# Kernel optimization log

Hardware: AMD Instinct MI355X
Metric: run time of the kernel (lower is better)

Reference implementation:

```python
import jax, jax.numpy as jnp
import numpy as np

B, H, S, D = 2, 16, 2048, 128  # batch, heads, seq_len, head_dim (hidden=2048, heads=16)


def setup_inputs() -> dict:
    key = jax.random.key(0)
    kq, kk, kv = jax.random.split(key, 3)
    q = jax.random.normal(kq, (B, H, S, D), dtype=jnp.float32)
    k = jax.random.normal(kk, (B, H, S, D), dtype=jnp.float32)
    v = jax.random.normal(kv, (B, H, S, D), dtype=jnp.float32)
    return {"q": q, "k": k, "v": v}


def reference(q, k, v):
    # scores = (q @ k^T) / sqrt(head_dim)  -> [B, H, S, S]
    scaling = 1.0 / jnp.sqrt(jnp.asarray(q.shape[-1], dtype=q.dtype))
    scores = jnp.einsum('bhqd,bhkd->bhqk', q, k) * scaling
    # softmax over keys (dropout p=0.0 -> identity in eval / p=0)
    weights = jax.nn.softmax(scores, axis=-1)
    # out = weights @ v -> [B, H, S, D]
    return jnp.einsum('bhqk,bhkd->bhqd', weights, v)
```

## Files before the change

### kernel.cpp

```cpp
#include <hip/hip_runtime.h>
#include <stdint.h>

typedef __attribute__((ext_vector_type(4))) float f32x4;
typedef __attribute__((ext_vector_type(16))) float f32x16;
typedef __attribute__((ext_vector_type(8))) short bf16x8;

constexpr int S_ = 2048;
constexpr int D_ = 128;
constexpr int BH = 32;
constexpr int KB = 64;
constexpr int NT = S_ / KB;
constexpr float QSCALE = 0.08838834764831845f * 1.4426950408889634f;

__device__ __forceinline__ short f2bf(float f) {
  uint32_t u = __float_as_uint(f);
  u += 0x7fffu + ((u >> 16) & 1u);
  return (short)(u >> 16);
}

__device__ __forceinline__ void gll16(const void* g, void* l) {
  __builtin_amdgcn_global_load_lds(
      (const __attribute__((address_space(1))) void*)g,
      (__attribute__((address_space(3))) void*)l, 16, 0, 0);
}

__global__ void prep_k(const float* __restrict__ k, short* __restrict__ kb) {
  const size_t N8 = (size_t)BH * S_ * D_ / 8;
  size_t i = (size_t)blockIdx.x * blockDim.x + threadIdx.x;
  const size_t stride = (size_t)gridDim.x * blockDim.x;
  for (; i < N8; i += stride) {
    float4 a = reinterpret_cast<const float4*>(k)[i * 2];
    float4 b = reinterpret_cast<const float4*>(k)[i * 2 + 1];
    bf16x8 o;
    o[0] = f2bf(a.x); o[1] = f2bf(a.y); o[2] = f2bf(a.z); o[3] = f2bf(a.w);
    o[4] = f2bf(b.x); o[5] = f2bf(b.y); o[6] = f2bf(b.z); o[7] = f2bf(b.w);
    reinterpret_cast<bf16x8*>(kb)[i] = o;
  }
}

__global__ void prep_vt(const float* __restrict__ v, short* __restrict__ vt) {
  __shared__ __align__(16) short Lt[64][136];
  const int bh = blockIdx.x >> 5;
  const int s0 = (blockIdx.x & 31) * 64;
  const int t = threadIdx.x;
#pragma unroll
  for (int i = 0; i < 4; ++i) {
    int g = t + 256 * i;
    int r = g >> 4, c8 = g & 15;
    const float* src = v + ((size_t)bh * S_ + s0 + r) * D_ + c8 * 8;
    float4 f0 = *reinterpret_cast<const float4*>(src);
    float4 f1 = *reinterpret_cast<const float4*>(src + 4);
    bf16x8 o;
    o[0] = f2bf(f0.x); o[1] = f2bf(f0.y); o[2] = f2bf(f0.z); o[3] = f2bf(f0.w);
    o[4] = f2bf(f1.x); o[5] = f2bf(f1.y); o[6] = f2bf(f1.z); o[7] = f2bf(f1.w);
    *reinterpret_cast<bf16x8*>(&Lt[r][c8 * 8]) = o;
  }
  __syncthreads();
#pragma unroll
  for (int i = 0; i < 4; ++i) {
    int g = t * 4 + i;
    int d = g >> 3, s8 = g & 7;
    bf16x8 o;
#pragma unroll
    for (int j = 0; j < 8; ++j) o[j] = Lt[s8 * 8 + j][d];
    *reinterpret_cast<bf16x8*>(&vt[((size_t)bh * D_ + d) * S_ + s0 + s8 * 8]) = o;
  }
}

__global__ __launch_bounds__(512, 2) void attn_fwd_v8(
    const float* __restrict__ q, const short* __restrict__ kbf,
    const short* __restrict__ vt, float* __restrict__ out)
{
  __shared__ __align__(16) short Klds[2][8192];
  __shared__ __align__(16) short Vlds[3][8192];

  const int lid = blockIdx.x;
  const int swz = (lid & 7) * 32 + (lid >> 3);
  const int qt = swz & 7;
  const int bh = swz >> 3;

  const int tid = threadIdx.x;
  const int wid = tid >> 6;
  const int lane = tid & 63;
  const int l32 = lane & 31;
  const int hi = lane >> 5;

  const int qrow = qt * 256 + wid * 32 + l32;

  bf16x8 bq[8];
  {
    const float* qg_ = q + ((size_t)bh * S_ + qrow) * D_ + hi * 8;
#pragma unroll
    for (int s = 0; s < 8; ++s) {
      float4 f0 = *reinterpret_cast<const float4*>(qg_ + s * 16);
      float4 f1 = *reinterpret_cast<const float4*>(qg_ + s * 16 + 4);
      bf16x8 a;
      a[0] = f2bf(f0.x * QSCALE); a[1] = f2bf(f0.y * QSCALE);
      a[2] = f2bf(f0.z * QSCALE); a[3] = f2bf(f0.w * QSCALE);
      a[4] = f2bf(f1.x * QSCALE); a[5] = f2bf(f1.y * QSCALE);
      a[6] = f2bf(f1.z * QSCALE); a[7] = f2bf(f1.w * QSCALE);
      bq[s] = a;
    }
  }

  const short* kg = kbf + (size_t)bh * S_ * D_;
  const short* vg = vt + (size_t)bh * D_ * S_;

  int kofs[2], vofs[2];
#pragma unroll
  for (int j = 0; j < 2; ++j) {
    const int g = wid * 2 + j;
    kofs[j] = lane * D_ + g * 8;
    const int G = g * 64 + lane;
    vofs[j] = (G & 127) * S_ + (G >> 7) * 8;
  }
  auto stage = [&](int t) {
    const short* ks = kg + (size_t)(t * KB) * D_;
    const short* vs = vg + t * KB;
    short* kd = &Klds[t & 1][wid * 1024];
    short* vd = &Vlds[t % 3][wid * 1024];
    gll16(ks + kofs[0], kd);
    gll16(ks + kofs[1], kd + 512);
    gll16(vs + vofs[0], vd);
    gll16(vs + vofs[1], vd + 512);
  };

  f32x16 oacc[4], loacc;
#pragma unroll
  for (int d0 = 0; d0 < 4; ++d0)
#pragma unroll
    for (int r = 0; r < 16; ++r) oacc[d0][r] = 0.f;
#pragma unroll
  for (int r = 0; r < 16; ++r) loacc[r] = 0.f;

  union { uint32_t u[4]; bf16x8 b; } onesu;
#pragma unroll
  for (int i = 0; i < 4; ++i) onesu.u[i] = 0x3F803F80u;

  bf16x8 pfrag[4];

  stage(0);
  for (int t = 0; t < NT; ++t) {
    __syncthreads();
    if (t + 1 < NT) stage(t + 1);

    const short* Kb = &Klds[t & 1][0];

    f32x16 sf0, sf1;
#pragma unroll
    for (int r = 0; r < 16; ++r) { sf0[r] = 0.f; sf1[r] = 0.f; }
    __builtin_amdgcn_s_setprio(1);
#pragma unroll
    for (int s = 0; s < 8; ++s) {
      bf16x8 a0 = *reinterpret_cast<const bf16x8*>(&Kb[((s * 2 + hi) * 64 + l32) * 8]);
      bf16x8 a1 = *reinterpret_cast<const bf16x8*>(&Kb[((s * 2 + hi) * 64 + 32 + l32) * 8]);
      sf0 = __builtin_amdgcn_mfma_f32_32x32x16_bf16(a0, bq[s], sf0, 0, 0, 0);
      sf1 = __builtin_amdgcn_mfma_f32_32x32x16_bf16(a1, bq[s], sf1, 0, 0, 0);
    }
    __builtin_amdgcn_s_setprio(0);

    if (t > 0) {
      const short* Vp = &Vlds[(t + 2) % 3][0];
      __builtin_amdgcn_s_setprio(1);
#pragma unroll
      for (int ks2 = 0; ks2 < 4; ++ks2) {
#pragma unroll
        for (int d0 = 0; d0 < 4; ++d0) {
          bf16x8 av = *reinterpret_cast<const bf16x8*>(
              &Vp[((ks2 * 2 + hi) * 128 + d0 * 32 + l32) * 8]);
          oacc[d0] = __builtin_amdgcn_mfma_f32_32x32x16_bf16(av, pfrag[ks2], oacc[d0], 0, 0, 0);
        }
        loacc = __builtin_amdgcn_mfma_f32_32x32x16_bf16(onesu.b, pfrag[ks2], loacc, 0, 0, 0);
      }
      __builtin_amdgcn_s_setprio(0);
    }

#define MAKE_P(SF, F0)                                                          \
    {                                                                           \
      uint32_t w[8];                                                            \
      _Pragma("unroll")                                                         \
      for (int i2 = 0; i2 < 8; ++i2) {                                          \
        float e0 = exp2f(SF[2 * i2]);                                           \
        float e1 = exp2f(SF[2 * i2 + 1]);                                       \
        asm("v_cvt_pk_bf16_f32 %0, %1, %2" : "=v"(w[i2]) : "v"(e0), "v"(e1));   \
      }                                                                         \
      asm("v_permlane32_swap_b32 %0, %1" : "+v"(w[0]), "+v"(w[2]));             \
      asm("v_permlane32_swap_b32 %0, %1" : "+v"(w[1]), "+v"(w[3]));             \
      asm("v_permlane32_swap_b32 %0, %1" : "+v"(w[4]), "+v"(w[6]));             \
      asm("v_permlane32_swap_b32 %0, %1" : "+v"(w[5]), "+v"(w[7]));             \
      union { int4 i4; bf16x8 b; } u0, u1;                                      \
      u0.i4 = (int4){(int)w[0], (int)w[1], (int)w[2], (int)w[3]};               \
      u1.i4 = (int4){(int)w[4], (int)w[5], (int)w[6], (int)w[7]};               \
      pfrag[F0] = u0.b; pfrag[F0 + 1] = u1.b;                                   \
    }
    MAKE_P(sf0, 0)
    MAKE_P(sf1, 2)
#undef MAKE_P
  }

  {
    const short* Vp = &Vlds[(NT - 1) % 3][0];
    __builtin_amdgcn_s_setprio(1);
#pragma unroll
    for (int ks2 = 0; ks2 < 4; ++ks2) {
#pragma unroll
      for (int d0 = 0; d0 < 4; ++d0) {
        bf16x8 av = *reinterpret_cast<const bf16x8*>(
            &Vp[((ks2 * 2 + hi) * 128 + d0 * 32 + l32) * 8]);
        oacc[d0] = __builtin_amdgcn_mfma_f32_32x32x16_bf16(av, pfrag[ks2], oacc[d0], 0, 0, 0);
      }
      loacc = __builtin_amdgcn_mfma_f32_32x32x16_bf16(onesu.b, pfrag[ks2], loacc, 0, 0, 0);
    }
    __builtin_amdgcn_s_setprio(0);
  }

  const float inv = 1.0f / loacc[0];
  float* ob = out + ((size_t)bh * S_ + qrow) * D_;
#pragma unroll
  for (int d0 = 0; d0 < 4; ++d0)
#pragma unroll
    for (int r2 = 0; r2 < 4; ++r2) {
      float4 o4 = {oacc[d0][r2 * 4 + 0] * inv, oacc[d0][r2 * 4 + 1] * inv,
                   oacc[d0][r2 * 4 + 2] * inv, oacc[d0][r2 * 4 + 3] * inv};
      *reinterpret_cast<float4*>(ob + d0 * 32 + r2 * 8 + hi * 4) = o4;
    }
}

__global__ __launch_bounds__(256, 4) void attn_fwd_v1(
    const float* __restrict__ q, const float* __restrict__ k,
    const float* __restrict__ v, float* __restrict__ out)
{
  __shared__ __align__(16) short Klds[32 * 128];
  __shared__ __align__(16) short Vlds[128 * 40];
  __shared__ __align__(16) short Plds[4][16 * 40];
  const int lid = blockIdx.x;
  const int swz = (lid & 7) * 128 + (lid >> 3);
  const int qt = swz & 31;
  const int bh = swz >> 5;
  const int tid = threadIdx.x;
  const int wid = tid >> 6;
  const int lane = tid & 63;
  const int l16 = lane & 15;
  const int lhi = lane >> 4;
  const int qrow0 = qt * 64 + wid * 16;
  const float* qg = q + ((size_t)bh * S_ + qrow0 + l16) * D_;
  const float* kg = k + (size_t)bh * S_ * D_;
  const float* vg = v + (size_t)bh * S_ * D_;
  bf16x8 aq[4];
#pragma unroll
  for (int ks = 0; ks < 4; ++ks) {
    const float* p = qg + ks * 32 + lhi * 8;
    float4 f0 = *reinterpret_cast<const float4*>(p);
    float4 f1 = *reinterpret_cast<const float4*>(p + 4);
    bf16x8 a;
    a[0] = f2bf(f0.x * QSCALE); a[1] = f2bf(f0.y * QSCALE);
    a[2] = f2bf(f0.z * QSCALE); a[3] = f2bf(f0.w * QSCALE);
    a[4] = f2bf(f1.x * QSCALE); a[5] = f2bf(f1.y * QSCALE);
    a[6] = f2bf(f1.z * QSCALE); a[7] = f2bf(f1.w * QSCALE);
    aq[ks] = a;
  }
  float mrow[4], lrow[4];
  f32x4 oacc[8];
#pragma unroll
  for (int r = 0; r < 4; ++r) { mrow[r] = -1e30f; lrow[r] = 0.f; }
#pragma unroll
  for (int i = 0; i < 8; ++i) oacc[i] = (f32x4){0.f, 0.f, 0.f, 0.f};
  for (int t = 0; t < S_ / 32; ++t) {
    const int kv0 = t * 32;
    __syncthreads();
#pragma unroll
    for (int i = 0; i < 2; ++i) {
      const int g = tid * 2 + i;
      const int row = g >> 4;
      const int c8 = g & 15;
      const float* ksrc = kg + (size_t)(kv0 + row) * D_ + c8 * 8;
      float4 f0 = *reinterpret_cast<const float4*>(ksrc);
      float4 f1 = *reinterpret_cast<const float4*>(ksrc + 4);
      bf16x8 kk;
      kk[0] = f2bf(f0.x); kk[1] = f2bf(f0.y); kk[2] = f2bf(f0.z); kk[3] = f2bf(f0.w);
      kk[4] = f2bf(f1.x); kk[5] = f2bf(f1.y); kk[6] = f2bf(f1.z); kk[7] = f2bf(f1.w);
      *reinterpret_cast<bf16x8*>(
          &Klds[row * D_ + ((c8 * 8) ^ ((row & 7) << 3))]) = kk;
      const float* vsrc = vg + (size_t)(kv0 + row) * D_ + c8 * 8;
      float4 g0 = *reinterpret_cast<const float4*>(vsrc);
      float4 g1 = *reinterpret_cast<const float4*>(vsrc + 4);
      const int dbase = c8 * 8;
      Vlds[(dbase + 0) * 40 + row] = f2bf(g0.x);
      Vlds[(dbase + 1) * 40 + row] = f2bf(g0.y);
      Vlds[(dbase + 2) * 40 + row] = f2bf(g0.z);
      Vlds[(dbase + 3) * 40 + row] = f2bf(g0.w);
      Vlds[(dbase + 4) * 40 + row] = f2bf(g1.x);
      Vlds[(dbase + 5) * 40 + row] = f2bf(g1.y);
      Vlds[(dbase + 6) * 40 + row] = f2bf(g1.z);
      Vlds[(dbase + 7) * 40 + row] = f2bf(g1.w);
    }
    __syncthreads();
    f32x4 sfrag[2];
#pragma unroll
    for (int kb = 0; kb < 2; ++kb) {
      f32x4 acc = (f32x4){0.f, 0.f, 0.f, 0.f};
#pragma unroll
      for (int ks = 0; ks < 4; ++ks) {
        const int rowk = kb * 16 + l16;
        bf16x8 bk = *reinterpret_cast<const bf16x8*>(
            &Klds[rowk * D_ + (((ks * 4 + lhi) * 8) ^ ((rowk & 7) << 3))]);
        acc = __builtin_amdgcn_mfma_f32_16x16x32_bf16(aq[ks], bk, acc, 0, 0, 0);
      }
      sfrag[kb] = acc;
    }
    float mt[4];
#pragma unroll
    for (int r = 0; r < 4; ++r) mt[r] = fmaxf(sfrag[0][r], sfrag[1][r]);
#pragma unroll
    for (int off = 1; off < 16; off <<= 1)
#pragma unroll
      for (int r = 0; r < 4; ++r) mt[r] = fmaxf(mt[r], __shfl_xor(mt[r], off, 64));
    float al[4], ps[4];
#pragma unroll
    for (int r = 0; r < 4; ++r) {
      float mn = fmaxf(mrow[r], mt[r]);
      al[r] = exp2f(mrow[r] - mn);
      mrow[r] = mn;
      ps[r] = 0.f;
    }
#pragma unroll
    for (int kb = 0; kb < 2; ++kb)
#pragma unroll
      for (int r = 0; r < 4; ++r) {
        float p = exp2f(sfrag[kb][r] - mrow[r]);
        ps[r] += p;
        Plds[wid][(lhi * 4 + r) * 40 + kb * 16 + l16] = f2bf(p);
      }
#pragma unroll
    for (int off = 1; off < 16; off <<= 1)
#pragma unroll
      for (int r = 0; r < 4; ++r) ps[r] += __shfl_xor(ps[r], off, 64);
#pragma unroll
    for (int r = 0; r < 4; ++r) lrow[r] = lrow[r] * al[r] + ps[r];
#pragma unroll
    for (int i = 0; i < 8; ++i)
#pragma unroll
      for (int r = 0; r < 4; ++r) oacc[i][r] *= al[r];
    bf16x8 ap = *reinterpret_cast<const bf16x8*>(&Plds[wid][l16 * 40 + lhi * 8]);
#pragma unroll
    for (int d0 = 0; d0 < 8; ++d0) {
      bf16x8 bv = *reinterpret_cast<const bf16x8*>(
          &Vlds[(d0 * 16 + l16) * 40 + lhi * 8]);
      oacc[d0] = __builtin_amdgcn_mfma_f32_16x16x32_bf16(ap, bv, oacc[d0], 0, 0, 0);
    }
  }
#pragma unroll
  for (int r = 0; r < 4; ++r) {
    float inv = 1.0f / lrow[r];
    float* orow = out + ((size_t)bh * S_ + qrow0 + lhi * 4 + r) * D_ + l16;
#pragma unroll
    for (int d0 = 0; d0 < 8; ++d0) orow[d0 * 16] = oacc[d0][r] * inv;
  }
}

extern "C" void kernel_launch(void* const* d_in, const int* in_sizes, int n_in,
                              void* d_out, int out_size, void* d_ws, size_t ws_size,
                              hipStream_t stream) {
  (void)in_sizes; (void)n_in; (void)out_size;
  const float* q = (const float*)d_in[0];
  const float* k = (const float*)d_in[1];
  const float* v = (const float*)d_in[2];
  float* o = (float*)d_out;
  const size_t NEL = (size_t)BH * S_ * D_;
  const size_t need = NEL * 2 * sizeof(short);
  if (ws_size >= need) {
    short* kb = (short*)d_ws;
    short* vt = kb + NEL;
    hipLaunchKernelGGL(prep_k, dim3(2048), dim3(256), 0, stream, k, kb);
    hipLaunchKernelGGL(prep_vt, dim3(1024), dim3(256), 0, stream, v, vt);
    hipLaunchKernelGGL(attn_fwd_v8, dim3(256), dim3(512), 0, stream, q, kb, vt, o);
  } else {
    hipLaunchKernelGGL(attn_fwd_v1, dim3(1024), dim3(256), 0, stream, q, k, v, o);
  }
}
```

Measured before the change: 126.0 us.

## Halve attention workgroups to 4 waves and stagger PV/QK order across waves

The attention kernel now runs 512 workgroups of 256 threads (4 waves, 128 query rows each) instead of 256 workgroups of 512 threads. Each wave issues twice as many async global-to-LDS loads per tile. The loop barrier is replaced by an explicit vmcnt(0) wait plus s_barrier with scheduling fences. Odd waves do the P·V MFMA block before the QK^T block and even waves after it, so matrix and exp work from different waves can interleave. In exchange, K/V tiles are loaded into LDS twice as often in total, since each workgroup covers fewer query rows, and LDS use per workgroup stays the same, which may limit occupancy.

```diff
diff --git a/kernel.cpp b/kernel.cpp
--- a/kernel.cpp
+++ b/kernel.cpp
@@ -67,7 +67,7 @@
   }
 }
 
-__global__ __launch_bounds__(512, 2) void attn_fwd_v8(
+__global__ __launch_bounds__(256, 2) void attn_fwd_v10(
     const float* __restrict__ q, const short* __restrict__ kbf,
     const short* __restrict__ vt, float* __restrict__ out)
 {
@@ -75,9 +75,9 @@
   __shared__ __align__(16) short Vlds[3][8192];
 
   const int lid = blockIdx.x;
-  const int swz = (lid & 7) * 32 + (lid >> 3);
-  const int qt = swz & 7;
-  const int bh = swz >> 3;
+  const int swz = (lid & 7) * 64 + (lid >> 3);
+  const int qt = swz & 15;
+  const int bh = swz >> 4;
 
   const int tid = threadIdx.x;
   const int wid = tid >> 6;
@@ -85,7 +85,7 @@
   const int l32 = lane & 31;
   const int hi = lane >> 5;
 
-  const int qrow = qt * 256 + wid * 32 + l32;
+  const int qrow = qt * 128 + wid * 32 + l32;
 
   bf16x8 bq[8];
   {
@@ -106,10 +106,10 @@
   const short* kg = kbf + (size_t)bh * S_ * D_;
   const short* vg = vt + (size_t)bh * D_ * S_;
 
-  int kofs[2], vofs[2];
-#pragma unroll
-  for (int j = 0; j < 2; ++j) {
-    const int g = wid * 2 + j;
+  int kofs[4], vofs[4];
+#pragma unroll
+  for (int j = 0; j < 4; ++j) {
+    const int g = wid * 4 + j;
     kofs[j] = lane * D_ + g * 8;
     const int G = g * 64 + lane;
     vofs[j] = (G & 127) * S_ + (G >> 7) * 8;
@@ -117,12 +117,12 @@
   auto stage = [&](int t) {
     const short* ks = kg + (size_t)(t * KB) * D_;
     const short* vs = vg + t * KB;
-    short* kd = &Klds[t & 1][wid * 1024];
-    short* vd = &Vlds[t % 3][wid * 1024];
-    gll16(ks + kofs[0], kd);
-    gll16(ks + kofs[1], kd + 512);
-    gll16(vs + vofs[0], vd);
-    gll16(vs + vofs[1], vd + 512);
+    short* kd = &Klds[t & 1][wid * 2048];
+    short* vd = &Vlds[t % 3][wid * 2048];
+#pragma unroll
+    for (int j = 0; j < 4; ++j) gll16(ks + kofs[j], kd + j * 512);
+#pragma unroll
+    for (int j = 0; j < 4; ++j) gll16(vs + vofs[j], vd + j * 512);
   };
 
   f32x16 oacc[4], loacc;
@@ -138,13 +138,36 @@
   for (int i = 0; i < 4; ++i) onesu.u[i] = 0x3F803F80u;
 
   bf16x8 pfrag[4];
+
+#define PV_BLOCK(VIDX)                                                          \
+  {                                                                             \
+    const short* Vp = &Vlds[(VIDX)][0];                                         \
+    __builtin_amdgcn_s_setprio(1);                                              \
+    _Pragma("unroll")                                                           \
+    for (int ks2 = 0; ks2 < 4; ++ks2) {                                         \
+      _Pragma("unroll")                                                         \
+      for (int d0 = 0; d0 < 4; ++d0) {                                          \
+        bf16x8 av = *reinterpret_cast<const bf16x8*>(                           \
+            &Vp[((ks2 * 2 + hi) * 128 + d0 * 32 + l32) * 8]);                   \
+        oacc[d0] = __builtin_amdgcn_mfma_f32_32x32x16_bf16(av, pfrag[ks2], oacc[d0], 0, 0, 0); \
+      }                                                                         \
+      loacc = __builtin_amdgcn_mfma_f32_32x32x16_bf16(onesu.b, pfrag[ks2], loacc, 0, 0, 0);    \
+    }                                                                           \
+    __builtin_amdgcn_s_setprio(0);                                              \
+  }
 
   stage(0);
   for (int t = 0; t < NT; ++t) {
-    __syncthreads();
+    __builtin_amdgcn_sched_barrier(0);
+    asm volatile("s_waitcnt vmcnt(0)" ::: "memory");
+    __builtin_amdgcn_sched_barrier(0);
+    __builtin_amdgcn_s_barrier();
+    __builtin_amdgcn_sched_barrier(0);
     if (t + 1 < NT) stage(t + 1);
 
     const short* Kb = &Klds[t & 1][0];
+
+    if ((wid & 1) && t > 0) PV_BLOCK((t + 2) % 3)
 
     f32x16 sf0, sf1;
 #pragma unroll
@@ -159,21 +182,7 @@
     }
     __builtin_amdgcn_s_setprio(0);
 
-    if (t > 0) {
-      const short* Vp = &Vlds[(t + 2) % 3][0];
-      __builtin_amdgcn_s_setprio(1);
-#pragma unroll
-      for (int ks2 = 0; ks2 < 4; ++ks2) {
-#pragma unroll
-        for (int d0 = 0; d0 < 4; ++d0) {
-          bf16x8 av = *reinterpret_cast<const bf16x8*>(
-              &Vp[((ks2 * 2 + hi) * 128 + d0 * 32 + l32) * 8]);
-          oacc[d0] = __builtin_amdgcn_mfma_f32_32x32x16_bf16(av, pfrag[ks2], oacc[d0], 0, 0, 0);
-        }
-        loacc = __builtin_amdgcn_mfma_f32_32x32x16_bf16(onesu.b, pfrag[ks2], loacc, 0, 0, 0);
-      }
-      __builtin_amdgcn_s_setprio(0);
-    }
+    if (!(wid & 1) && t > 0) PV_BLOCK((t + 2) % 3)
 
 #define MAKE_P(SF, F0)                                                          \
     {                                                                           \
@@ -198,21 +207,8 @@
 #undef MAKE_P
   }
 
-  {
-    const short* Vp = &Vlds[(NT - 1) % 3][0];
-    __builtin_amdgcn_s_setprio(1);
-#pragma unroll
-    for (int ks2 = 0; ks2 < 4; ++ks2) {
-#pragma unroll
-      for (int d0 = 0; d0 < 4; ++d0) {
-        bf16x8 av = *reinterpret_cast<const bf16x8*>(
-            &Vp[((ks2 * 2 + hi) * 128 + d0 * 32 + l32) * 8]);
-        oacc[d0] = __builtin_amdgcn_mfma_f32_32x32x16_bf16(av, pfrag[ks2], oacc[d0], 0, 0, 0);
-      }
-      loacc = __builtin_amdgcn_mfma_f32_32x32x16_bf16(onesu.b, pfrag[ks2], loacc, 0, 0, 0);
-    }
-    __builtin_amdgcn_s_setprio(0);
-  }
+  PV_BLOCK((NT - 1) % 3)
+#undef PV_BLOCK
 
   const float inv = 1.0f / loacc[0];
   float* ob = out + ((size_t)bh * S_ + qrow) * D_;
@@ -373,7 +369,7 @@
     short* vt = kb + NEL;
     hipLaunchKernelGGL(prep_k, dim3(2048), dim3(256), 0, stream, k, kb);
     hipLaunchKernelGGL(prep_vt, dim3(1024), dim3(256), 0, stream, v, vt);
-    hipLaunchKernelGGL(attn_fwd_v8, dim3(256), dim3(512), 0, stream, q, kb, vt, o);
+    hipLaunchKernelGGL(attn_fwd_v10, dim3(512), dim3(256), 0, stream, q, kb, vt, o);
   } else {
     hipLaunchKernelGGL(attn_fwd_v1, dim3(1024), dim3(256), 0, stream, q, k, v, o);
   }
```

Result: faster. 118.8 us (-5.7%).

## Replace LDS-staged K/V pipeline with direct global loads into MFMA operands

Applied to the files above, without the earlier changes.

Removes the shared-memory double/triple buffering of K and V tiles, the global_load_lds staging and the per-iteration block barrier. Each wave now loads its K and transposed-V fragments straight from global memory (relying on L2/L1 reuse across the 8 waves), and the PV MFMA moves from the next iteration into the same iteration as the softmax. Launch bounds drop to one block per SM, allowing more registers. The cost is that inter-wave data reuse now depends on caches rather than LDS, global load latency is exposed, and the software pipelining between QK and PV is lost.

```diff
diff --git a/kernel.cpp b/kernel.cpp
--- a/kernel.cpp
+++ b/kernel.cpp
@@ -16,12 +16,6 @@
   uint32_t u = __float_as_uint(f);
   u += 0x7fffu + ((u >> 16) & 1u);
   return (short)(u >> 16);
-}
-
-__device__ __forceinline__ void gll16(const void* g, void* l) {
-  __builtin_amdgcn_global_load_lds(
-      (const __attribute__((address_space(1))) void*)g,
-      (__attribute__((address_space(3))) void*)l, 16, 0, 0);
 }
 
 __global__ void prep_k(const float* __restrict__ k, short* __restrict__ kb) {
@@ -67,13 +61,10 @@
   }
 }
 
-__global__ __launch_bounds__(512, 2) void attn_fwd_v8(
+__global__ __launch_bounds__(512, 1) void attn_fwd_v11(
     const float* __restrict__ q, const short* __restrict__ kbf,
     const short* __restrict__ vt, float* __restrict__ out)
 {
-  __shared__ __align__(16) short Klds[2][8192];
-  __shared__ __align__(16) short Vlds[3][8192];
-
   const int lid = blockIdx.x;
   const int swz = (lid & 7) * 32 + (lid >> 3);
   const int qt = swz & 7;
@@ -103,27 +94,8 @@
     }
   }
 
-  const short* kg = kbf + (size_t)bh * S_ * D_;
-  const short* vg = vt + (size_t)bh * D_ * S_;
-
-  int kofs[2], vofs[2];
-#pragma unroll
-  for (int j = 0; j < 2; ++j) {
-    const int g = wid * 2 + j;
-    kofs[j] = lane * D_ + g * 8;
-    const int G = g * 64 + lane;
-    vofs[j] = (G & 127) * S_ + (G >> 7) * 8;
-  }
-  auto stage = [&](int t) {
-    const short* ks = kg + (size_t)(t * KB) * D_;
-    const short* vs = vg + t * KB;
-    short* kd = &Klds[t & 1][wid * 1024];
-    short* vd = &Vlds[t % 3][wid * 1024];
-    gll16(ks + kofs[0], kd);
-    gll16(ks + kofs[1], kd + 512);
-    gll16(vs + vofs[0], vd);
-    gll16(vs + vofs[1], vd + 512);
-  };
+  const short* kp = kbf + (size_t)bh * S_ * D_ + (size_t)l32 * D_ + hi * 8;
+  const short* vp = vt + (size_t)bh * D_ * S_ + (size_t)l32 * S_ + hi * 8;
 
   f32x16 oacc[4], loacc;
 #pragma unroll
@@ -137,14 +109,9 @@
 #pragma unroll
   for (int i = 0; i < 4; ++i) onesu.u[i] = 0x3F803F80u;
 
-  bf16x8 pfrag[4];
-
-  stage(0);
   for (int t = 0; t < NT; ++t) {
-    __syncthreads();
-    if (t + 1 < NT) stage(t + 1);
-
-    const short* Kb = &Klds[t & 1][0];
+    const short* kt = kp + (size_t)t * KB * D_;
+    const short* vcol = vp + (size_t)t * KB;
 
     f32x16 sf0, sf1;
 #pragma unroll
@@ -152,29 +119,14 @@
     __builtin_amdgcn_s_setprio(1);
 #pragma unroll
     for (int s = 0; s < 8; ++s) {
-      bf16x8 a0 = *reinterpret_cast<const bf16x8*>(&Kb[((s * 2 + hi) * 64 + l32) * 8]);
-      bf16x8 a1 = *reinterpret_cast<const bf16x8*>(&Kb[((s * 2 + hi) * 64 + 32 + l32) * 8]);
+      bf16x8 a0 = *reinterpret_cast<const bf16x8*>(kt + s * 16);
+      bf16x8 a1 = *reinterpret_cast<const bf16x8*>(kt + 32 * D_ + s * 16);
       sf0 = __builtin_amdgcn_mfma_f32_32x32x16_bf16(a0, bq[s], sf0, 0, 0, 0);
       sf1 = __builtin_amdgcn_mfma_f32_32x32x16_bf16(a1, bq[s], sf1, 0, 0, 0);
     }
     __builtin_amdgcn_s_setprio(0);
 
-    if (t > 0) {
-      const short* Vp = &Vlds[(t + 2) % 3][0];
-      __builtin_amdgcn_s_setprio(1);
-#pragma unroll
-      for (int ks2 = 0; ks2 < 4; ++ks2) {
-#pragma unroll
-        for (int d0 = 0; d0 < 4; ++d0) {
-          bf16x8 av = *reinterpret_cast<const bf16x8*>(
-              &Vp[((ks2 * 2 + hi) * 128 + d0 * 32 + l32) * 8]);
-          oacc[d0] = __builtin_amdgcn_mfma_f32_32x32x16_bf16(av, pfrag[ks2], oacc[d0], 0, 0, 0);
-        }
-        loacc = __builtin_amdgcn_mfma_f32_32x32x16_bf16(onesu.b, pfrag[ks2], loacc, 0, 0, 0);
-      }
-      __builtin_amdgcn_s_setprio(0);
-    }
-
+    bf16x8 pfrag[4];
 #define MAKE_P(SF, F0)                                                          \
     {                                                                           \
       uint32_t w[8];                                                            \
@@ -196,17 +148,14 @@
     MAKE_P(sf0, 0)
     MAKE_P(sf1, 2)
 #undef MAKE_P
-  }
-
-  {
-    const short* Vp = &Vlds[(NT - 1) % 3][0];
+
     __builtin_amdgcn_s_setprio(1);
 #pragma unroll
     for (int ks2 = 0; ks2 < 4; ++ks2) {
+      const short* vc = vcol + (size_t)ks2 * 16;
 #pragma unroll
       for (int d0 = 0; d0 < 4; ++d0) {
-        bf16x8 av = *reinterpret_cast<const bf16x8*>(
-            &Vp[((ks2 * 2 + hi) * 128 + d0 * 32 + l32) * 8]);
+        bf16x8 av = *reinterpret_cast<const bf16x8*>(vc + (size_t)d0 * 32 * S_);
         oacc[d0] = __builtin_amdgcn_mfma_f32_32x32x16_bf16(av, pfrag[ks2], oacc[d0], 0, 0, 0);
       }
       loacc = __builtin_amdgcn_mfma_f32_32x32x16_bf16(onesu.b, pfrag[ks2], loacc, 0, 0, 0);
@@ -373,7 +322,7 @@
     short* vt = kb + NEL;
     hipLaunchKernelGGL(prep_k, dim3(2048), dim3(256), 0, stream, k, kb);
     hipLaunchKernelGGL(prep_vt, dim3(1024), dim3(256), 0, stream, v, vt);
-    hipLaunchKernelGGL(attn_fwd_v8, dim3(256), dim3(512), 0, stream, q, kb, vt, o);
+    hipLaunchKernelGGL(attn_fwd_v11, dim3(256), dim3(512), 0, stream, q, kb, vt, o);
   } else {
     hipLaunchKernelGGL(attn_fwd_v1, dim3(1024), dim3(256), 0, stream, q, k, v, o);
   }
```

Measured after the change: 266.3 us. 111% more time.
